# Performance work log

Measured on AMD Instinct MI355X. Metric: run time of the kernel, lower is better.

The kernel has to match this reference:

```python
import jax, jax.numpy as jnp
import numpy as np

NUM_TREES = 150
ARITY = 4
DEPTH = 4
NUM_LEVELS = DEPTH + 1  # leaves (level 0) ... root (level DEPTH)
VOCAB = 10000
SUBTOK = 8
EMB_DIM = 256
HID = 256
NUM_CLASSES = 2


def _build_forest():
    # perfect ARITY-ary tree, level-order indexing; edges point child -> parent
    n = (ARITY ** (DEPTH + 1) - 1) // (ARITY - 1)  # 341
    src = np.arange(1, n)
    dst = (src - 1) // ARITY
    depth_of = np.zeros(n, dtype=np.int64)
    for j in range(1, n):
        depth_of[j] = depth_of[(j - 1) // ARITY] + 1
    level_of = DEPTH - depth_of  # leaves = 0, processed first (topo order)
    offs = np.arange(NUM_TREES) * n
    edge_src = (src[None, :] + offs[:, None]).ravel().astype(np.int32)
    edge_dst = (dst[None, :] + offs[:, None]).ravel().astype(np.int32)
    node_level = np.tile(level_of, NUM_TREES).astype(np.int32)
    graph_id = np.repeat(np.arange(NUM_TREES), n).astype(np.int32)
    leaf_mask = (node_level == 0).astype(np.int32)
    return edge_src, edge_dst, node_level, graph_id, leaf_mask, NUM_TREES * n


def setup_inputs() -> dict:
    key = jax.random.key(0)
    ks = jax.random.split(key, 16)
    es, ed, lvl, gid, lm, N = _build_forest()
    s_e = 1.0 / np.sqrt(EMB_DIM)
    s_h = 1.0 / np.sqrt(HID)
    s_f = 1.0 / np.sqrt(2 * HID)
    return {
        "node_feat1": jax.random.randint(ks[0], (N, SUBTOK), 0, VOCAB, dtype=jnp.int32),
        "node_feat2": jax.random.randint(ks[1], (N, SUBTOK), 0, VOCAB, dtype=jnp.int32),
        "emb1": jax.random.normal(ks[2], (VOCAB, EMB_DIM), jnp.float32) * 0.02,
        "emb2": jax.random.normal(ks[3], (VOCAB, EMB_DIM), jnp.float32) * 0.02,
        "W_iou1": jax.random.normal(ks[4], (EMB_DIM, 3 * HID), jnp.float32) * s_e,
        "W_iou2": jax.random.normal(ks[5], (EMB_DIM, 3 * HID), jnp.float32) * s_e,
        "U_iou1": jax.random.normal(ks[6], (HID, 3 * HID), jnp.float32) * s_h,
        "U_iou2": jax.random.normal(ks[7], (HID, 3 * HID), jnp.float32) * s_h,
        "Uf_W1": jax.random.normal(ks[8], (HID, HID), jnp.float32) * s_h,
        "Uf_b1": jnp.zeros((HID,), jnp.float32),
        "Uf_W2": jax.random.normal(ks[9], (HID, HID), jnp.float32) * s_h,
        "Uf_b2": jnp.zeros((HID,), jnp.float32),
        "b_iou1": jnp.zeros((3 * HID,), jnp.float32),
        "b_iou2": jnp.zeros((3 * HID,), jnp.float32),
        "Wf": jax.random.normal(ks[10], (2 * HID, NUM_CLASSES), jnp.float32) * s_f,
        "bf": jnp.zeros((NUM_CLASSES,), jnp.float32),
        "edge_src": jnp.asarray(es),
        "edge_dst": jnp.asarray(ed),
        "node_level": jnp.asarray(lvl),
        "graph_id": jnp.asarray(gid),
        "leaf_mask": jnp.asarray(lm),
    }


def _tree_lstm(iou0, U_iou, Uf_W, Uf_b, b_iou, edge_src, edge_dst, node_level):
    # ChildSum TreeLSTM, propagated level-by-level (leaves -> root)
    N = iou0.shape[0]
    h = jnp.zeros((N, HID), iou0.dtype)
    c = jnp.zeros((N, HID), iou0.dtype)
    for lvl in range(NUM_LEVELS):
        emask = (node_level[edge_dst] == lvl).astype(h.dtype)[:, None]  # [E,1]
        hs = h[edge_src] * emask  # children h (already computed at lower levels)
        f = jax.nn.sigmoid(hs @ Uf_W + Uf_b)  # per-edge forget gate
        h_tild = jax.ops.segment_sum(hs, edge_dst, num_segments=N)
        c_sum = jax.ops.segment_sum(f * c[edge_src] * emask, edge_dst, num_segments=N)
        has_child = jax.ops.segment_sum(emask, edge_dst, num_segments=N) > 0  # [N,1]
        # DGL semantics: reduce overwrites iou for internal nodes; leaves keep W_iou(x)*mask
        iou = jnp.where(has_child, h_tild @ U_iou, iou0) + b_iou
        i, o, u = jnp.split(iou, 3, axis=1)
        c_new = jax.nn.sigmoid(i) * jnp.tanh(u) + c_sum
        h_new = jax.nn.sigmoid(o) * jnp.tanh(c_new)
        at = (node_level == lvl)[:, None]
        h = jnp.where(at, h_new, h)
        c = jnp.where(at, c_new, c)
    return h


def _branch(node_feat, emb, W_iou, U_iou, Uf_W, Uf_b, b_iou,
            leaf_mask, edge_src, edge_dst, node_level, graph_id):
    embeds = emb[node_feat].mean(axis=1)  # subtoken mean pooling -> [N, EMB_DIM]
    iou0 = (embeds @ W_iou) * leaf_mask.astype(embeds.dtype)[:, None]
    h = _tree_lstm(iou0, U_iou, Uf_W, Uf_b, b_iou, edge_src, edge_dst, node_level)
    s = jax.ops.segment_sum(h, graph_id, num_segments=NUM_TREES)
    cnt = jax.ops.segment_sum(jnp.ones((h.shape[0],), h.dtype), graph_id, num_segments=NUM_TREES)
    return jax.nn.relu(s / cnt[:, None])  # mean graph readout + relu


def reference(node_feat1, node_feat2, emb1, emb2, W_iou1, W_iou2, U_iou1, U_iou2,
              Uf_W1, Uf_b1, Uf_W2, Uf_b2, b_iou1, b_iou2, Wf, bf,
              edge_src, edge_dst, node_level, graph_id, leaf_mask):
    m1 = _branch(node_feat1, emb1, W_iou1, U_iou1, Uf_W1, Uf_b1, b_iou1,
                 leaf_mask, edge_src, edge_dst, node_level, graph_id)
    m2 = _branch(node_feat2, emb2, W_iou2, U_iou2, Uf_W2, Uf_b2, b_iou2,
                 leaf_mask, edge_src, edge_dst, node_level, graph_id)
    logits = jax.nn.leaky_relu(jnp.concatenate([m1, m2], axis=1) @ Wf + bf, 0.01)
    return jax.nn.softmax(logits, axis=-1)
```

## Files before the change

kernel.cpp:

```cpp
#include <hip/hip_runtime.h>

#define NT 150
#define NPT 341
#define LEAF0 85
#define NL (NT*256)
#define NN (NT*NPT)
#define VOCAB 10000

typedef __attribute__((ext_vector_type(8))) short short8;
typedef __attribute__((ext_vector_type(4))) float floatx4;

__device__ __forceinline__ float sigf(float x){
  return __builtin_amdgcn_rcpf(1.0f + __expf(-x));
}
__device__ __forceinline__ float tanh_fast(float x){
  float e = __expf(2.0f*x);
  return 1.0f - 2.0f*__builtin_amdgcn_rcpf(e + 1.0f);
}
__device__ __forceinline__ float bf2f(ushort u){ union{unsigned i; float f;} v; v.i = ((unsigned)u)<<16; return v.f; }
__device__ __forceinline__ ushort f2bf(float x){ union{float f; unsigned i;} v; v.f = x; return (ushort)((v.i + 0x7fff + ((v.i>>16)&1))>>16); }

__global__ __launch_bounds__(256) void prep_k(
    const float* __restrict__ e1, const float* __restrict__ e2,
    ushort* __restrict__ E1, ushort* __restrict__ E2,
    const float* __restrict__ W1, const float* __restrict__ U1, const float* __restrict__ F1,
    const float* __restrict__ W2, const float* __restrict__ U2, const float* __restrict__ F2,
    ushort* Wt1, ushort* Ut1, ushort* Ft1, ushort* Wt2, ushort* Ut2, ushort* Ft2){
  __shared__ float T[32][33];
  int bid = blockIdx.x;
  if (bid < 5000){
    const float* s = (bid >= 2500) ? e2 : e1;
    ushort* d = (bid >= 2500) ? E2 : E1;
    size_t i = ((size_t)(bid % 2500)*256 + threadIdx.x)*4;
    float4 v = *(const float4*)&s[i];
    d[i+0]=f2bf(v.x); d[i+1]=f2bf(v.y); d[i+2]=f2bf(v.z); d[i+3]=f2bf(v.w);
    return;
  }
  int w = bid - 5000;
  int z = w / 192, rem = w % 192;
  int bx = rem % 24, by = rem / 24;
  const float* src; ushort* dst; int N;
  switch (z){
    case 0: src=W1; dst=Wt1; N=768; break;
    case 1: src=U1; dst=Ut1; N=768; break;
    case 2: src=F1; dst=Ft1; N=256; break;
    case 3: src=W2; dst=Wt2; N=768; break;
    case 4: src=U2; dst=Ut2; N=768; break;
    default: src=F2; dst=Ft2; N=256; break;
  }
  int n0 = bx*32; if (n0 >= N) return;
  int k0 = by*32;
  int nl = threadIdx.x & 31, kb = threadIdx.x >> 5;
  #pragma unroll
  for (int i=0;i<4;i++){ int kk = kb*4+i; T[kk][nl] = src[(size_t)(k0+kk)*N + n0 + nl]; }
  __syncthreads();
  #pragma unroll
  for (int i=0;i<4;i++){ int nn = kb*4+i; dst[(size_t)(n0+nn)*256 + k0 + nl] = f2bf(T[nl][nn]); }
}

__global__ __launch_bounds__(1024, 4) void leaf_lvl1_k(
    const int* __restrict__ f1, const int* __restrict__ f2,
    const ushort* __restrict__ E1, const ushort* __restrict__ E2,
    const ushort* __restrict__ Wt1, const ushort* __restrict__ Ut1,
    const ushort* __restrict__ Ft1, const float* __restrict__ b1,
    const float* __restrict__ Ufb1,
    const ushort* __restrict__ Wt2, const ushort* __restrict__ Ut2,
    const ushort* __restrict__ Ft2, const float* __restrict__ b2,
    const float* __restrict__ Ufb2,
    ushort* __restrict__ h1, ushort* __restrict__ c1,
    ushort* __restrict__ h2, ushort* __restrict__ c2){
  __shared__ __attribute__((aligned(16))) ushort As[8][64*40];
  int br = blockIdx.y;
  const int* feat = br ? f2 : f1;
  const ushort* E = br ? E2 : E1;
  const ushort* Wt = br ? Wt2 : Wt1;
  const ushort* Ut = br ? Ut2 : Ut1;
  const ushort* Ft = br ? Ft2 : Ft1;
  const float* biou = br ? b2 : b1;
  const float* Ufb = br ? Ufb2 : Ufb1;
  ushort* h = br ? h2 : h1;
  ushort* c = br ? c2 : c1;
  int tid = threadIdx.x;
  int lane = tid & 63, wav = tid >> 6, quad = lane >> 4, l15 = lane & 15;
  int rowbase = blockIdx.x*64;
  int tree = rowbase >> 8, lbase = rowbase & 255;
  size_t tb = (size_t)tree*NPT;

  {
    int row = tid >> 4, seg = tid & 15;
    size_t node = tb + LEAF0 + lbase + row;
    const int* f = feat + node*8;
    int4 fA = *(const int4*)f;
    int4 fB = *(const int4*)(f+4);
    int idx[8] = {fA.x, fA.y, fA.z, fA.w, fB.x, fB.y, fB.z, fB.w};
    float s[16];
    #pragma unroll
    for (int q=0;q<16;q++) s[q]=0.f;
    #pragma unroll
    for (int half=0; half<2; half++){
      short8 va[4], vb[4];
      #pragma unroll
      for (int j=0;j<4;j++){
        const ushort* rowp = E + (size_t)idx[half*4+j]*256 + seg*16;
        va[j] = *(const short8*)rowp;
        vb[j] = *(const short8*)(rowp+8);
      }
      #pragma unroll
      for (int j=0;j<4;j++){
        #pragma unroll
        for (int q=0;q<8;q++){ s[q]+=bf2f((ushort)va[j][q]); s[8+q]+=bf2f((ushort)vb[j][q]); }
      }
    }
    short8 o1, o2;
    #pragma unroll
    for (int q=0;q<8;q++){ o1[q]=(short)f2bf(s[q]*0.125f); o2[q]=(short)f2bf(s[8+q]*0.125f); }
    int cch = seg >> 1, off = (seg & 1)*16;
    *(short8*)&As[cch][row*40 + off]     = o1;
    *(short8*)&As[cch][row*40 + off + 8] = o2;
  }
  __syncthreads();

  floatx4 acc[3][4];
  #pragma unroll
  for (int g=0;g<3;g++)
    #pragma unroll
    for (int r=0;r<4;r++) acc[g][r] = (floatx4){0.f,0.f,0.f,0.f};

  int hc = wav*16 + l15;
  const ushort* bp0 = Wt + (size_t)(0*256 + hc)*256 + quad*8;
  const ushort* bp1 = Wt + (size_t)(256 + hc)*256 + quad*8;
  const ushort* bp2 = Wt + (size_t)(512 + hc)*256 + quad*8;

  #pragma unroll
  for (int cch=0; cch<8; cch++){
    short8 b0 = *(const short8*)(bp0 + cch*32);
    short8 b1 = *(const short8*)(bp1 + cch*32);
    short8 b2 = *(const short8*)(bp2 + cch*32);
    #pragma unroll
    for (int r=0;r<4;r++){
      short8 a = *(const short8*)&As[cch][(16*r + l15)*40 + quad*8];
      acc[0][r] = __builtin_amdgcn_mfma_f32_16x16x32_bf16(a, b0, acc[0][r], 0,0,0);
      acc[1][r] = __builtin_amdgcn_mfma_f32_16x16x32_bf16(a, b1, acc[1][r], 0,0,0);
      acc[2][r] = __builtin_amdgcn_mfma_f32_16x16x32_bf16(a, b2, acc[2][r], 0,0,0);
    }
  }
  __syncthreads();

  float bi = biou[hc], bo = biou[256+hc], bu = biou[512+hc];
  float cv[16];
  #pragma unroll
  for (int r=0;r<4;r++){
    #pragma unroll
    for (int reg=0;reg<4;reg++){
      int row = 16*r + quad*4 + reg;
      float iv = acc[0][r][reg] + bi;
      float ov = acc[1][r][reg] + bo;
      float uv = acc[2][r][reg] + bu;
      float cc = sigf(iv)*tanh_fast(uv);
      float hh = sigf(ov)*tanh_fast(cc);
      cv[4*r+reg] = cc;
      ushort hb = f2bf(hh);
      h[(tb + LEAF0 + lbase + row)*256 + hc] = hb;
      As[hc>>5][row*40 + (hc & 31)] = hb;
    }
  }
  __syncthreads();

  const ushort* bfp = Ft + (size_t)hc*256 + quad*8;
  const ushort* up0 = Ut + (size_t)(0*256 + hc)*256 + quad*8;
  const ushort* up1 = Ut + (size_t)(256 + hc)*256 + quad*8;
  const ushort* up2 = Ut + (size_t)(512 + hc)*256 + quad*8;

  floatx4 af[4], ai[4], ao[4], au[4];
  #pragma unroll
  for (int r=0;r<4;r++){
    af[r] = (floatx4){0.f,0.f,0.f,0.f}; ai[r] = (floatx4){0.f,0.f,0.f,0.f};
    ao[r] = (floatx4){0.f,0.f,0.f,0.f}; au[r] = (floatx4){0.f,0.f,0.f,0.f};
  }
  #pragma unroll
  for (int cch=0; cch<8; cch++){
    short8 Bf = *(const short8*)(bfp + cch*32);
    short8 Bi = *(const short8*)(up0 + cch*32);
    short8 Bo = *(const short8*)(up1 + cch*32);
    short8 Bu = *(const short8*)(up2 + cch*32);
    #pragma unroll
    for (int r=0;r<4;r++){
      short8 a = *(const short8*)&As[cch][(16*r + l15)*40 + quad*8];
      af[r] = __builtin_amdgcn_mfma_f32_16x16x32_bf16(a, Bf, af[r], 0,0,0);
      ai[r] = __builtin_amdgcn_mfma_f32_16x16x32_bf16(a, Bi, ai[r], 0,0,0);
      ao[r] = __builtin_amdgcn_mfma_f32_16x16x32_bf16(a, Bo, ao[r], 0,0,0);
      au[r] = __builtin_amdgcn_mfma_f32_16x16x32_bf16(a, Bu, au[r], 0,0,0);
    }
  }

  int nodebase = 21 + (lbase >> 2);
  float ufb = Ufb[hc];
  float bI = biou[hc], bO = biou[256+hc], bU = biou[512+hc];
  #pragma unroll
  for (int r=0;r<4;r++){
    int m_local = 4*r + quad;
    float cs = 0.f;
    #pragma unroll
    for (int reg=0;reg<4;reg++)
      cs += sigf(af[r][reg] + ufb) * cv[4*r+reg];
    float iv = ai[r][0]+ai[r][1]+ai[r][2]+ai[r][3] + bI;
    float ov = ao[r][0]+ao[r][1]+ao[r][2]+ao[r][3] + bO;
    float uv = au[r][0]+au[r][1]+au[r][2]+au[r][3] + bU;
    float cn = sigf(iv)*tanh_fast(uv) + cs;
    float hn = sigf(ov)*tanh_fast(cn);
    size_t off = (tb + nodebase + m_local)*256 + hc;
    h[off] = f2bf(hn);
    c[off] = f2bf(cn);
  }
}

__global__ __launch_bounds__(512) void level_k(
    const ushort* __restrict__ Ut1, const ushort* __restrict__ Ft1,
    const float* __restrict__ Ufb1, const float* __restrict__ bi1,
    const ushort* __restrict__ Ut2, const ushort* __restrict__ Ft2,
    const float* __restrict__ Ufb2, const float* __restrict__ bi2,
    ushort* __restrict__ h1, ushort* __restrict__ c1,
    ushort* __restrict__ h2, ushort* __restrict__ c2,
    int M, int shift, int base){
  __shared__ __attribute__((aligned(16))) ushort Ch[8][64*40];
  int br = blockIdx.z;
  const ushort* Ut = br ? Ut2 : Ut1;
  const ushort* Ft = br ? Ft2 : Ft1;
  const float* Ufb = br ? Ufb2 : Ufb1;
  const float* biou = br ? bi2 : bi1;
  ushort* h = br ? h2 : h1;
  ushort* c = br ? c2 : c1;
  int tid = threadIdx.x;
  int lane = tid & 63, wav = tid >> 6, quad = lane >> 4, l15 = lane & 15;
  int m0 = blockIdx.x*16;
  int mask = (1<<shift)-1;

  {
    int cl = tid >> 3, s8 = tid & 7;
    int sm = m0 + (cl >> 2); if (sm > M-1) sm = M-1;
    int stree = sm >> shift, sloc = base + (sm & mask);
    const ushort* sgp = h + ((size_t)stree*NPT + 4*sloc + 1 + (cl & 3))*256 + s8*32;
    short8 v0 = *(const short8*)(sgp);
    short8 v1 = *(const short8*)(sgp+8);
    short8 v2 = *(const short8*)(sgp+16);
    short8 v3 = *(const short8*)(sgp+24);
    *(short8*)&Ch[s8][cl*40 + 0]  = v0;
    *(short8*)&Ch[s8][cl*40 + 8]  = v1;
    *(short8*)&Ch[s8][cl*40 + 16] = v2;
    *(short8*)&Ch[s8][cl*40 + 24] = v3;
  }
  __syncthreads();

  int col = blockIdx.y*128 + wav*16 + l15;
  const ushort* bfp = Ft + (size_t)col*256 + quad*8;
  const ushort* bp0 = Ut + (size_t)(0*256 + col)*256 + quad*8;
  const ushort* bp1 = Ut + (size_t)(256 + col)*256 + quad*8;
  const ushort* bp2 = Ut + (size_t)(512 + col)*256 + quad*8;

  floatx4 af[4], ai[4], ao[4], au[4];
  #pragma unroll
  for (int r=0;r<4;r++){
    af[r] = (floatx4){0.f,0.f,0.f,0.f}; ai[r] = (floatx4){0.f,0.f,0.f,0.f};
    ao[r] = (floatx4){0.f,0.f,0.f,0.f}; au[r] = (floatx4){0.f,0.f,0.f,0.f};
  }

  #pragma unroll
  for (int cc=0; cc<8; cc++){
    short8 Bf = *(const short8*)(bfp + cc*32);
    short8 Bi = *(const short8*)(bp0 + cc*32);
    short8 Bo = *(const short8*)(bp1 + cc*32);
    short8 Bu = *(const short8*)(bp2 + cc*32);
    #pragma unroll
    for (int r=0;r<4;r++){
      short8 a = *(const short8*)&Ch[cc][(16*r + l15)*40 + quad*8];
      af[r] = __builtin_amdgcn_mfma_f32_16x16x32_bf16(a, Bf, af[r], 0,0,0);
      ai[r] = __builtin_amdgcn_mfma_f32_16x16x32_bf16(a, Bi, ai[r], 0,0,0);
      ao[r] = __builtin_amdgcn_mfma_f32_16x16x32_bf16(a, Bo, ao[r], 0,0,0);
      au[r] = __builtin_amdgcn_mfma_f32_16x16x32_bf16(a, Bu, au[r], 0,0,0);
    }
  }

  float ufb = Ufb[col];
  float bI = biou[col], bO = biou[256+col], bU = biou[512+col];
  #pragma unroll
  for (int r=0;r<4;r++){
    int m = m0 + 4*r + quad;
    int mm = m < M ? m : M-1;
    int tree = mm >> shift, loc = base + (mm & mask);
    size_t ch0 = ((size_t)tree*NPT + 4*loc + 1)*256 + col;
    float cs = 0.f;
    #pragma unroll
    for (int reg=0;reg<4;reg++)
      cs += sigf(af[r][reg] + ufb) * bf2f(c[ch0 + (size_t)reg*256]);
    float iv = ai[r][0]+ai[r][1]+ai[r][2]+ai[r][3] + bI;
    float ov = ao[r][0]+ao[r][1]+ao[r][2]+ao[r][3] + bO;
    float uv = au[r][0]+au[r][1]+au[r][2]+au[r][3] + bU;
    float cn = sigf(iv)*tanh_fast(uv) + cs;
    float hn = sigf(ov)*tanh_fast(cn);
    if (m < M){
      size_t off = ((size_t)tree*NPT + loc)*256 + col;
      h[off] = f2bf(hn);
      c[off] = f2bf(cn);
    }
  }
}

__global__ __launch_bounds__(256) void readout_k(
    const ushort* __restrict__ h1, const ushort* __restrict__ h2,
    float* __restrict__ mp1, float* __restrict__ mp2){
  __shared__ float red[4][256];
  int br = blockIdx.z, part = blockIdx.y, tree = blockIdx.x;
  const ushort* h = br ? h2 : h1;
  float* mp = br ? mp2 : mp1;
  int t = threadIdx.x;
  int lane = t & 63, rg = t >> 6;
  int start = part*85;
  int cnt = (part==3) ? 86 : 85;
  const ushort* base = h + ((size_t)tree*NPT + start)*256 + lane*4;
  float s0=0.f,s1=0.f,s2=0.f,s3=0.f;
  for (int i=rg; i<cnt; i+=4){
    ushort4 v = *(const ushort4*)(base + (size_t)i*256);
    s0 += bf2f(v.x); s1 += bf2f(v.y); s2 += bf2f(v.z); s3 += bf2f(v.w);
  }
  *(float4*)&red[rg][lane*4] = make_float4(s0,s1,s2,s3);
  __syncthreads();
  float tot = red[0][t]+red[1][t]+red[2][t]+red[3][t];
  mp[((size_t)tree*4 + part)*256 + t] = tot;
}

__global__ __launch_bounds__(64) void final_k(const float* __restrict__ mp1,
    const float* __restrict__ mp2, const float* __restrict__ Wf,
    const float* __restrict__ bf, float* __restrict__ out){
  int tree = blockIdx.x; int t = threadIdx.x;
  float p0=0.f, p1=0.f;
  for (int k=t;k<512;k+=64){
    const float* mp = (k<256) ? mp1 : mp2;
    int kk = k & 255;
    size_t b0 = ((size_t)tree*4)*256 + kk;
    float s = mp[b0] + mp[b0+256] + mp[b0+512] + mp[b0+768];
    float x = fmaxf(s*(1.0f/341.0f), 0.f);
    p0 += x*Wf[k*2+0]; p1 += x*Wf[k*2+1];
  }
  #pragma unroll
  for (int off=32; off>0; off>>=1){
    p0 += __shfl_down(p0, off);
    p1 += __shfl_down(p1, off);
  }
  if (t==0){
    float l0 = p0+bf[0], l1 = p1+bf[1];
    l0 = (l0>0.f)?l0:0.01f*l0;
    l1 = (l1>0.f)?l1:0.01f*l1;
    float mx = fmaxf(l0,l1);
    float e0 = __expf(l0-mx), e1 = __expf(l1-mx);
    float inv = 1.0f/(e0+e1);
    out[tree*2+0] = e0*inv; out[tree*2+1] = e1*inv;
  }
}

extern "C" void kernel_launch(void* const* d_in, const int* in_sizes, int n_in,
                              void* d_out, int out_size, void* d_ws, size_t ws_size,
                              hipStream_t stream) {
  const int*   feat1 = (const int*)  d_in[0];
  const int*   feat2 = (const int*)  d_in[1];
  const float* emb1  = (const float*)d_in[2];
  const float* emb2  = (const float*)d_in[3];
  const float* Wiou1 = (const float*)d_in[4];
  const float* Wiou2 = (const float*)d_in[5];
  const float* Uiou1 = (const float*)d_in[6];
  const float* Uiou2 = (const float*)d_in[7];
  const float* UfW1  = (const float*)d_in[8];
  const float* Ufb1  = (const float*)d_in[9];
  const float* UfW2  = (const float*)d_in[10];
  const float* Ufb2  = (const float*)d_in[11];
  const float* biou1 = (const float*)d_in[12];
  const float* biou2 = (const float*)d_in[13];
  const float* Wf    = (const float*)d_in[14];
  const float* bfv   = (const float*)d_in[15];
  float* out = (float*)d_out;

  char* ws = (char*)d_ws;
  ushort* h1  = (ushort*)ws;  ws += (size_t)NN*256*2;
  ushort* h2  = (ushort*)ws;  ws += (size_t)NN*256*2;
  ushort* c1  = (ushort*)ws;  ws += (size_t)NN*256*2;
  ushort* c2  = (ushort*)ws;  ws += (size_t)NN*256*2;
  ushort* E1  = (ushort*)ws;  ws += (size_t)VOCAB*256*2;
  ushort* E2  = (ushort*)ws;  ws += (size_t)VOCAB*256*2;
  ushort* Wt1 = (ushort*)ws;  ws += 768*256*2;
  ushort* Ut1 = (ushort*)ws;  ws += 768*256*2;
  ushort* Ft1 = (ushort*)ws;  ws += 256*256*2;
  ushort* Wt2 = (ushort*)ws;  ws += 768*256*2;
  ushort* Ut2 = (ushort*)ws;  ws += 768*256*2;
  ushort* Ft2 = (ushort*)ws;  ws += 256*256*2;
  float*  mp1 = (float*)ws;   ws += (size_t)NT*4*256*4;
  float*  mp2 = (float*)ws;   ws += (size_t)NT*4*256*4;

  prep_k<<<dim3(6152), 256, 0, stream>>>(emb1, emb2, E1, E2,
                                         Wiou1, Uiou1, UfW1, Wiou2, Uiou2, UfW2,
                                         Wt1, Ut1, Ft1, Wt2, Ut2, Ft2);
  leaf_lvl1_k<<<dim3(NL/64, 2), 1024, 0, stream>>>(feat1, feat2, E1, E2,
                                                   Wt1, Ut1, Ft1, biou1, Ufb1,
                                                   Wt2, Ut2, Ft2, biou2, Ufb2,
                                                   h1, c1, h2, c2);

  const int lvlM[3]     = {2400, 600, 150};
  const int lvlShift[3] = {4, 2, 0};
  const int lvlBase[3]  = {5, 1, 0};
  for (int l=0;l<3;l++){
    int gx = (lvlM[l] + 15)/16;
    level_k<<<dim3(gx, 2, 2), 512, 0, stream>>>(Ut1, Ft1, Ufb1, biou1,
                                                Ut2, Ft2, Ufb2, biou2,
                                                h1, c1, h2, c2,
                                                lvlM[l], lvlShift[l], lvlBase[l]);
  }
  readout_k<<<dim3(NT, 4, 2), 256, 0, stream>>>(h1, h2, mp1, mp2);
  final_k<<<NT, 64, 0, stream>>>(mp1, mp2, Wf, bfv, out);
}
```

Baseline: 367.4 us.

## Fuse upper tree levels and readout into one per-tree kernel

Replaces the three per-level launches and the separate readout kernel with a single tree_k kernel, one block per tree and branch. Levels 2-4 are computed in that block with hidden and cell states kept in LDS, and the graph sum is accumulated in registers plus a read of the lower-level h values. The leaf kernel now writes h with vectorized row stores from LDS instead of scattered 2-byte stores. This removes launch overhead and the global round-trips between levels. In exchange only 300 blocks run, and the small upper levels use one MFMA row tile per wave, so parallelism is limited.

```diff
diff --git a/kernel.cpp b/kernel.cpp
--- a/kernel.cpp
+++ b/kernel.cpp
@@ -159,12 +159,18 @@
       float cc = sigf(iv)*tanh_fast(uv);
       float hh = sigf(ov)*tanh_fast(cc);
       cv[4*r+reg] = cc;
-      ushort hb = f2bf(hh);
-      h[(tb + LEAF0 + lbase + row)*256 + hc] = hb;
-      As[hc>>5][row*40 + (hc & 31)] = hb;
-    }
-  }
-  __syncthreads();
+      As[hc>>5][row*40 + (hc & 31)] = f2bf(hh);
+    }
+  }
+  __syncthreads();
+
+  {
+    int row = tid >> 4, seg = tid & 15;
+    const ushort* sp = &As[seg>>1][row*40 + (seg & 1)*16];
+    ushort* dp = h + (tb + LEAF0 + lbase + row)*256 + seg*16;
+    *(short8*)dp = *(const short8*)sp;
+    *(short8*)(dp+8) = *(const short8*)(sp+8);
+  }
 
   const ushort* bfp = Ft + (size_t)hc*256 + quad*8;
   const ushort* up0 = Ut + (size_t)(0*256 + hc)*256 + quad*8;
@@ -214,48 +220,49 @@
   }
 }
 
-__global__ __launch_bounds__(512) void level_k(
+__global__ __launch_bounds__(1024, 4) void tree_k(
     const ushort* __restrict__ Ut1, const ushort* __restrict__ Ft1,
     const float* __restrict__ Ufb1, const float* __restrict__ bi1,
     const ushort* __restrict__ Ut2, const ushort* __restrict__ Ft2,
     const float* __restrict__ Ufb2, const float* __restrict__ bi2,
-    ushort* __restrict__ h1, ushort* __restrict__ c1,
-    ushort* __restrict__ h2, ushort* __restrict__ c2,
-    int M, int shift, int base){
+    const ushort* __restrict__ h1, const ushort* __restrict__ c1,
+    const ushort* __restrict__ h2, const ushort* __restrict__ c2,
+    float* __restrict__ mp1, float* __restrict__ mp2){
   __shared__ __attribute__((aligned(16))) ushort Ch[8][64*40];
-  int br = blockIdx.z;
+  __shared__ ushort C2b[16][256];
+  __shared__ ushort C3b[4][256];
+  __shared__ float RS[4][256];
+  int br = blockIdx.y, tree = blockIdx.x;
   const ushort* Ut = br ? Ut2 : Ut1;
   const ushort* Ft = br ? Ft2 : Ft1;
   const float* Ufb = br ? Ufb2 : Ufb1;
   const float* biou = br ? bi2 : bi1;
-  ushort* h = br ? h2 : h1;
-  ushort* c = br ? c2 : c1;
+  const ushort* h = br ? h2 : h1;
+  const ushort* c = br ? c2 : c1;
+  float* mp = br ? mp2 : mp1;
   int tid = threadIdx.x;
   int lane = tid & 63, wav = tid >> 6, quad = lane >> 4, l15 = lane & 15;
-  int m0 = blockIdx.x*16;
-  int mask = (1<<shift)-1;
+  int hc = wav*16 + l15;
+  size_t tb = (size_t)tree*NPT;
 
   {
-    int cl = tid >> 3, s8 = tid & 7;
-    int sm = m0 + (cl >> 2); if (sm > M-1) sm = M-1;
-    int stree = sm >> shift, sloc = base + (sm & mask);
-    const ushort* sgp = h + ((size_t)stree*NPT + 4*sloc + 1 + (cl & 3))*256 + s8*32;
-    short8 v0 = *(const short8*)(sgp);
-    short8 v1 = *(const short8*)(sgp+8);
-    short8 v2 = *(const short8*)(sgp+16);
-    short8 v3 = *(const short8*)(sgp+24);
-    *(short8*)&Ch[s8][cl*40 + 0]  = v0;
-    *(short8*)&Ch[s8][cl*40 + 8]  = v1;
-    *(short8*)&Ch[s8][cl*40 + 16] = v2;
-    *(short8*)&Ch[s8][cl*40 + 24] = v3;
-  }
-  __syncthreads();
-
-  int col = blockIdx.y*128 + wav*16 + l15;
-  const ushort* bfp = Ft + (size_t)col*256 + quad*8;
-  const ushort* bp0 = Ut + (size_t)(0*256 + col)*256 + quad*8;
-  const ushort* bp1 = Ut + (size_t)(256 + col)*256 + quad*8;
-  const ushort* bp2 = Ut + (size_t)(512 + col)*256 + quad*8;
+    int row = tid >> 4, seg = tid & 15;
+    const ushort* sp = h + (tb + 21 + row)*256 + seg*16;
+    short8 a = *(const short8*)sp;
+    short8 b = *(const short8*)(sp+8);
+    int cch = seg >> 1, off = (seg & 1)*16;
+    *(short8*)&Ch[cch][row*40 + off]     = a;
+    *(short8*)&Ch[cch][row*40 + off + 8] = b;
+  }
+  __syncthreads();
+
+  const ushort* bfp = Ft + (size_t)hc*256 + quad*8;
+  const ushort* up0 = Ut + (size_t)(0*256 + hc)*256 + quad*8;
+  const ushort* up1 = Ut + (size_t)(256 + hc)*256 + quad*8;
+  const ushort* up2 = Ut + (size_t)(512 + hc)*256 + quad*8;
+  float ufb = Ufb[hc];
+  float bI = biou[hc], bO = biou[256+hc], bU = biou[512+hc];
+  float rsum = 0.f;
 
   floatx4 af[4], ai[4], ao[4], au[4];
   #pragma unroll
@@ -263,69 +270,123 @@
     af[r] = (floatx4){0.f,0.f,0.f,0.f}; ai[r] = (floatx4){0.f,0.f,0.f,0.f};
     ao[r] = (floatx4){0.f,0.f,0.f,0.f}; au[r] = (floatx4){0.f,0.f,0.f,0.f};
   }
-
-  #pragma unroll
-  for (int cc=0; cc<8; cc++){
-    short8 Bf = *(const short8*)(bfp + cc*32);
-    short8 Bi = *(const short8*)(bp0 + cc*32);
-    short8 Bo = *(const short8*)(bp1 + cc*32);
-    short8 Bu = *(const short8*)(bp2 + cc*32);
+  #pragma unroll
+  for (int cch=0; cch<8; cch++){
+    short8 Bf = *(const short8*)(bfp + cch*32);
+    short8 Bi = *(const short8*)(up0 + cch*32);
+    short8 Bo = *(const short8*)(up1 + cch*32);
+    short8 Bu = *(const short8*)(up2 + cch*32);
     #pragma unroll
     for (int r=0;r<4;r++){
-      short8 a = *(const short8*)&Ch[cc][(16*r + l15)*40 + quad*8];
+      short8 a = *(const short8*)&Ch[cch][(16*r + l15)*40 + quad*8];
       af[r] = __builtin_amdgcn_mfma_f32_16x16x32_bf16(a, Bf, af[r], 0,0,0);
       ai[r] = __builtin_amdgcn_mfma_f32_16x16x32_bf16(a, Bi, ai[r], 0,0,0);
       ao[r] = __builtin_amdgcn_mfma_f32_16x16x32_bf16(a, Bo, ao[r], 0,0,0);
       au[r] = __builtin_amdgcn_mfma_f32_16x16x32_bf16(a, Bu, au[r], 0,0,0);
     }
   }
-
-  float ufb = Ufb[col];
-  float bI = biou[col], bO = biou[256+col], bU = biou[512+col];
-  #pragma unroll
-  for (int r=0;r<4;r++){
-    int m = m0 + 4*r + quad;
-    int mm = m < M ? m : M-1;
-    int tree = mm >> shift, loc = base + (mm & mask);
-    size_t ch0 = ((size_t)tree*NPT + 4*loc + 1)*256 + col;
+  __syncthreads();
+  ushort h2v[4], c2v[4];
+  #pragma unroll
+  for (int r=0;r<4;r++){
+    int m = 4*r + quad;
     float cs = 0.f;
     #pragma unroll
     for (int reg=0;reg<4;reg++)
-      cs += sigf(af[r][reg] + ufb) * bf2f(c[ch0 + (size_t)reg*256]);
+      cs += sigf(af[r][reg] + ufb) * bf2f(c[(tb + 21 + 4*m + reg)*256 + hc]);
     float iv = ai[r][0]+ai[r][1]+ai[r][2]+ai[r][3] + bI;
     float ov = ao[r][0]+ao[r][1]+ao[r][2]+ao[r][3] + bO;
     float uv = au[r][0]+au[r][1]+au[r][2]+au[r][3] + bU;
     float cn = sigf(iv)*tanh_fast(uv) + cs;
     float hn = sigf(ov)*tanh_fast(cn);
-    if (m < M){
-      size_t off = ((size_t)tree*NPT + loc)*256 + col;
-      h[off] = f2bf(hn);
-      c[off] = f2bf(cn);
-    }
-  }
-}
-
-__global__ __launch_bounds__(256) void readout_k(
-    const ushort* __restrict__ h1, const ushort* __restrict__ h2,
-    float* __restrict__ mp1, float* __restrict__ mp2){
-  __shared__ float red[4][256];
-  int br = blockIdx.z, part = blockIdx.y, tree = blockIdx.x;
-  const ushort* h = br ? h2 : h1;
-  float* mp = br ? mp2 : mp1;
-  int t = threadIdx.x;
-  int lane = t & 63, rg = t >> 6;
-  int start = part*85;
-  int cnt = (part==3) ? 86 : 85;
-  const ushort* base = h + ((size_t)tree*NPT + start)*256 + lane*4;
-  float s0=0.f,s1=0.f,s2=0.f,s3=0.f;
-  for (int i=rg; i<cnt; i+=4){
-    ushort4 v = *(const ushort4*)(base + (size_t)i*256);
-    s0 += bf2f(v.x); s1 += bf2f(v.y); s2 += bf2f(v.z); s3 += bf2f(v.w);
-  }
-  *(float4*)&red[rg][lane*4] = make_float4(s0,s1,s2,s3);
-  __syncthreads();
-  float tot = red[0][t]+red[1][t]+red[2][t]+red[3][t];
-  mp[((size_t)tree*4 + part)*256 + t] = tot;
+    rsum += hn;
+    h2v[r] = f2bf(hn); c2v[r] = f2bf(cn);
+  }
+  #pragma unroll
+  for (int r=0;r<4;r++){
+    int m = 4*r + quad;
+    Ch[hc>>5][m*40 + (hc & 31)] = h2v[r];
+    C2b[m][hc] = c2v[r];
+  }
+  __syncthreads();
+
+  floatx4 f3 = (floatx4){0.f,0.f,0.f,0.f}, i3 = f3, o3 = f3, u3 = f3;
+  #pragma unroll
+  for (int cch=0; cch<8; cch++){
+    short8 Bf = *(const short8*)(bfp + cch*32);
+    short8 Bi = *(const short8*)(up0 + cch*32);
+    short8 Bo = *(const short8*)(up1 + cch*32);
+    short8 Bu = *(const short8*)(up2 + cch*32);
+    short8 a = *(const short8*)&Ch[cch][l15*40 + quad*8];
+    f3 = __builtin_amdgcn_mfma_f32_16x16x32_bf16(a, Bf, f3, 0,0,0);
+    i3 = __builtin_amdgcn_mfma_f32_16x16x32_bf16(a, Bi, i3, 0,0,0);
+    o3 = __builtin_amdgcn_mfma_f32_16x16x32_bf16(a, Bo, o3, 0,0,0);
+    u3 = __builtin_amdgcn_mfma_f32_16x16x32_bf16(a, Bu, u3, 0,0,0);
+  }
+  __syncthreads();
+  {
+    int q = quad;
+    float cs = 0.f;
+    #pragma unroll
+    for (int reg=0;reg<4;reg++)
+      cs += sigf(f3[reg] + ufb) * bf2f(C2b[4*q + reg][hc]);
+    float iv = i3[0]+i3[1]+i3[2]+i3[3] + bI;
+    float ov = o3[0]+o3[1]+o3[2]+o3[3] + bO;
+    float uv = u3[0]+u3[1]+u3[2]+u3[3] + bU;
+    float cn = sigf(iv)*tanh_fast(uv) + cs;
+    float hn = sigf(ov)*tanh_fast(cn);
+    rsum += hn;
+    Ch[hc>>5][q*40 + (hc & 31)] = f2bf(hn);
+    C3b[q][hc] = f2bf(cn);
+  }
+  __syncthreads();
+
+  floatx4 f4 = (floatx4){0.f,0.f,0.f,0.f}, i4 = f4, o4 = f4, u4 = f4;
+  #pragma unroll
+  for (int cch=0; cch<8; cch++){
+    short8 Bf = *(const short8*)(bfp + cch*32);
+    short8 Bi = *(const short8*)(up0 + cch*32);
+    short8 Bo = *(const short8*)(up1 + cch*32);
+    short8 Bu = *(const short8*)(up2 + cch*32);
+    short8 a = *(const short8*)&Ch[cch][l15*40 + quad*8];
+    f4 = __builtin_amdgcn_mfma_f32_16x16x32_bf16(a, Bf, f4, 0,0,0);
+    i4 = __builtin_amdgcn_mfma_f32_16x16x32_bf16(a, Bi, i4, 0,0,0);
+    o4 = __builtin_amdgcn_mfma_f32_16x16x32_bf16(a, Bo, o4, 0,0,0);
+    u4 = __builtin_amdgcn_mfma_f32_16x16x32_bf16(a, Bu, u4, 0,0,0);
+  }
+  if (quad == 0){
+    float cs = 0.f;
+    #pragma unroll
+    for (int reg=0;reg<4;reg++)
+      cs += sigf(f4[reg] + ufb) * bf2f(C3b[reg][hc]);
+    float iv = i4[0]+i4[1]+i4[2]+i4[3] + bI;
+    float ov = o4[0]+o4[1]+o4[2]+o4[3] + bO;
+    float uv = u4[0]+u4[1]+u4[2]+u4[3] + bU;
+    float cn = sigf(iv)*tanh_fast(uv) + cs;
+    float hn = sigf(ov)*tanh_fast(cn);
+    rsum += hn;
+  }
+  RS[quad][hc] = rsum;
+  __syncthreads();
+
+  float* red = (float*)&Ch[0][0];
+  {
+    int c4 = (tid & 63)*4, grp = tid >> 6;
+    const ushort* bp = h + (tb + 21)*256 + c4;
+    float s0=0.f,s1=0.f,s2=0.f,s3=0.f;
+    for (int i=grp; i<320; i+=16){
+      ushort4 v = *(const ushort4*)(bp + (size_t)i*256);
+      s0 += bf2f(v.x); s1 += bf2f(v.y); s2 += bf2f(v.z); s3 += bf2f(v.w);
+    }
+    *(float4*)&red[grp*256 + c4] = make_float4(s0,s1,s2,s3);
+  }
+  __syncthreads();
+  if (tid < 256){
+    float tot = RS[0][tid] + RS[1][tid] + RS[2][tid] + RS[3][tid];
+    #pragma unroll
+    for (int g=0; g<16; g++) tot += red[g*256 + tid];
+    mp[(size_t)tree*256 + tid] = tot;
+  }
 }
 
 __global__ __launch_bounds__(64) void final_k(const float* __restrict__ mp1,
@@ -336,8 +397,7 @@
   for (int k=t;k<512;k+=64){
     const float* mp = (k<256) ? mp1 : mp2;
     int kk = k & 255;
-    size_t b0 = ((size_t)tree*4)*256 + kk;
-    float s = mp[b0] + mp[b0+256] + mp[b0+512] + mp[b0+768];
+    float s = mp[(size_t)tree*256 + kk];
     float x = fmaxf(s*(1.0f/341.0f), 0.f);
     p0 += x*Wf[k*2+0]; p1 += x*Wf[k*2+1];
   }
@@ -401,17 +461,8 @@
                                                    Wt1, Ut1, Ft1, biou1, Ufb1,
                                                    Wt2, Ut2, Ft2, biou2, Ufb2,
                                                    h1, c1, h2, c2);
-
-  const int lvlM[3]     = {2400, 600, 150};
-  const int lvlShift[3] = {4, 2, 0};
-  const int lvlBase[3]  = {5, 1, 0};
-  for (int l=0;l<3;l++){
-    int gx = (lvlM[l] + 15)/16;
-    level_k<<<dim3(gx, 2, 2), 512, 0, stream>>>(Ut1, Ft1, Ufb1, biou1,
-                                                Ut2, Ft2, Ufb2, biou2,
-                                                h1, c1, h2, c2,
-                                                lvlM[l], lvlShift[l], lvlBase[l]);
-  }
-  readout_k<<<dim3(NT, 4, 2), 256, 0, stream>>>(h1, h2, mp1, mp2);
+  tree_k<<<dim3(NT, 2), 1024, 0, stream>>>(Ut1, Ft1, Ufb1, biou1,
+                                           Ut2, Ft2, Ufb2, biou2,
+                                           h1, c1, h2, c2, mp1, mp2);
   final_k<<<NT, 64, 0, stream>>>(mp1, mp2, Wf, bfv, out);
 }
```

Result: slower. 408.7 us (+11.2%).
